# Performance work log

Measured on AMD Instinct MI355X. Metric: run time of the kernel, lower is better.

The kernel has to match this reference:

```python
import jax, jax.numpy as jnp
import numpy as np

N = 50000
E = 1600000
D_IN = 512   # embedding_num - 1
D_OUT = 512  # output1_dim


def setup_inputs() -> dict:
    key = jax.random.key(0)
    ks = jax.random.split(key, 16)
    A1_tensor = jax.random.normal(ks[0], (N, D_IN + 1), dtype=jnp.float32)
    adj_rows = jax.random.randint(ks[1], (E,), 0, N, dtype=jnp.int32)
    adj_cols = jax.random.randint(ks[2], (E,), 0, N, dtype=jnp.int32)
    adj_vals = jax.random.uniform(ks[3], (E,), dtype=jnp.float32)
    s = 1.0 / np.sqrt(D_IN)
    Lin1 = jax.random.uniform(ks[4], (D_IN, D_OUT), minval=-s, maxval=s, dtype=jnp.float32)
    Lin1_bias = jax.random.uniform(ks[5], (D_OUT,), minval=-s, maxval=s, dtype=jnp.float32)
    n = jax.random.uniform(ks[6], (N, 1), minval=0.0, maxval=1.0, dtype=jnp.float32)
    W1 = jax.random.uniform(ks[7], (D_IN, D_OUT), minval=-s, maxval=s, dtype=jnp.float32)
    b1 = jax.random.uniform(ks[8], (D_OUT,), minval=-s, maxval=s, dtype=jnp.float32)
    s2 = 1.0 / np.sqrt(D_OUT)
    W2 = jax.random.uniform(ks[9], (D_OUT, D_OUT), minval=-s2, maxval=s2, dtype=jnp.float32)
    b2 = jax.random.uniform(ks[10], (D_OUT,), minval=-s2, maxval=s2, dtype=jnp.float32)
    W3 = jax.random.uniform(ks[11], (D_OUT, D_OUT), minval=-s2, maxval=s2, dtype=jnp.float32)
    b3 = jax.random.uniform(ks[12], (D_OUT,), minval=-s2, maxval=s2, dtype=jnp.float32)
    return {"A1_tensor": A1_tensor, "adj_rows": adj_rows, "adj_cols": adj_cols,
            "adj_vals": adj_vals, "Lin1": Lin1, "Lin1_bias": Lin1_bias, "n": n,
            "W1": W1, "b1": b1, "W2": W2, "b2": b2, "W3": W3, "b3": b3}


def reference(A1_tensor, adj_rows, adj_cols, adj_vals, Lin1, Lin1_bias, n,
              W1, b1, W2, b2, W3, b3):
    num_nodes = A1_tensor.shape[0]

    def spmm(h):  # sparse adj @ h via edge-list gather + segment_sum
        return jax.ops.segment_sum(adj_vals[:, None] * h[adj_cols], adj_rows,
                                   num_segments=num_nodes)

    x = A1_tensor[:, 1:]                      # drop first feature column (dropout = identity at eval)
    a0 = x @ Lin1 + Lin1_bias                 # [N, D_OUT]
    a1 = a0 * n
    x1 = spmm(x @ W1 + b1)                    # gc1
    x1 = a1 + x1 * (1.0 - n)                  # gated blend
    x2 = spmm(x1 @ W2 + b2)                   # gc2
    x2 = spmm(x2 @ W3 + b3)                   # gc3
    return jnp.concatenate([x2, a0], axis=-1) # [N, 2*D_OUT]
```

## Files before the change

kernel.cpp:

```cpp
#include <hip/hip_runtime.h>
#include <stdint.h>

#define DD 512

typedef __bf16 bf16x8 __attribute__((ext_vector_type(8)));
typedef float f32x4 __attribute__((ext_vector_type(4)));

__device__ __forceinline__ unsigned short f2bf(float f) {
  uint32_t u = __builtin_bit_cast(uint32_t, f);
  u += 0x7fff + ((u >> 16) & 1);
  return (unsigned short)(u >> 16);
}
__device__ __forceinline__ float bfbits2f(uint32_t lo16) {
  return __builtin_bit_cast(float, lo16 << 16);
}

__global__ void hist_kernel(const int* __restrict__ rows, int* __restrict__ counts, int E) {
  int i = blockIdx.x * blockDim.x + threadIdx.x;
  if (i < E) atomicAdd(&counts[rows[i]], 1);
}

__global__ __launch_bounds__(256) void scan_block(const int* __restrict__ counts,
                                                  int* __restrict__ offs, int* __restrict__ bsum,
                                                  int n) {
  __shared__ int sm[256];
  int t = threadIdx.x;
  int i = blockIdx.x * 256 + t;
  int v = (i < n) ? ((counts[i] + 7) & ~7) : 0;
  sm[t] = v;
  __syncthreads();
  for (int o = 1; o < 256; o <<= 1) {
    int x = (t >= o) ? sm[t - o] : 0;
    __syncthreads();
    sm[t] += x;
    __syncthreads();
  }
  if (i < n) offs[i + 1] = sm[t];
  if (t == 255) bsum[blockIdx.x] = sm[255];
}

__global__ __launch_bounds__(256) void scan_tops(int* __restrict__ bsum, int nb) {
  __shared__ int sm[256];
  int t = threadIdx.x;
  int v = (t < nb) ? bsum[t] : 0;
  sm[t] = v;
  __syncthreads();
  for (int o = 1; o < 256; o <<= 1) {
    int x = (t >= o) ? sm[t - o] : 0;
    __syncthreads();
    sm[t] += x;
    __syncthreads();
  }
  if (t < nb) bsum[t] = sm[t];
}

__global__ __launch_bounds__(256) void scan_add(int* __restrict__ offs,
                                                const int* __restrict__ bsum, int n) {
  int i = blockIdx.x * 256 + threadIdx.x;
  int add = (blockIdx.x > 0) ? bsum[blockIdx.x - 1] : 0;
  if (i < n) offs[i + 1] += add;
  if (i == 0) offs[0] = 0;
}

__global__ void scatter_kernel(const int* __restrict__ rows, const int* __restrict__ colsIn,
                               const float* __restrict__ valsIn, const int* __restrict__ offs,
                               int* __restrict__ cursor, int* __restrict__ colsC,
                               unsigned short* __restrict__ valsC, int E) {
  int i = blockIdx.x * blockDim.x + threadIdx.x;
  if (i < E) {
    int r = rows[i];
    int p = offs[r] + atomicAdd(&cursor[r], 1);
    colsC[p] = colsIn[i];
    valsC[p] = f2bf(valsIn[i]);
  }
}

__global__ __launch_bounds__(256) void convert_x(const float* __restrict__ A1,
                                                 __bf16* __restrict__ Xb, int N) {
  int id = blockIdx.x * 256 + threadIdx.x;
  int total = (N * DD) >> 3;
  if (id >= total) return;
  int r = id >> 6;
  int c = (id & 63) * 8;
  const float* p = A1 + (size_t)r * 513 + 1 + c;
  unsigned short h[8];
#pragma unroll
  for (int k = 0; k < 8; ++k) h[k] = f2bf(p[k]);
  uint4 o;
  o.x = (uint32_t)h[0] | ((uint32_t)h[1] << 16);
  o.y = (uint32_t)h[2] | ((uint32_t)h[3] << 16);
  o.z = (uint32_t)h[4] | ((uint32_t)h[5] << 16);
  o.w = (uint32_t)h[6] | ((uint32_t)h[7] << 16);
  *(uint4*)(Xb + (size_t)r * DD + c) = o;
}

__global__ __launch_bounds__(256) void convert_wt(const float* __restrict__ W,
                                                  __bf16* __restrict__ Wt) {
  __shared__ float tile[32][33];
  int bx = blockIdx.x * 32;
  int by = blockIdx.y * 32;
  int tx = threadIdx.x & 31, ty = threadIdx.x >> 5;
#pragma unroll
  for (int q = 0; q < 4; ++q)
    tile[ty + q * 8][tx] = W[(size_t)(by + ty + q * 8) * DD + bx + tx];
  __syncthreads();
  unsigned short* Wts = (unsigned short*)Wt;
#pragma unroll
  for (int q = 0; q < 4; ++q)
    Wts[(size_t)(bx + ty + q * 8) * DD + by + tx] = f2bf(tile[tx][ty + q * 8]);
}

template <int MODE>
__global__ __launch_bounds__(256) void gemm_mfma(
    const __bf16* __restrict__ A,
    const __bf16* __restrict__ Bt,
    const float* __restrict__ bias,
    __bf16* __restrict__ Yb,
    float* __restrict__ out,
    const float* __restrict__ nvec,
    int M) {
  __shared__ __bf16 As[128][64];
  __shared__ __bf16 Bs[128][64];
  const int tid = threadIdx.x;
  const int bx = blockIdx.x >> 2;
  const int by = blockIdx.x & 3;
  const int bm = bx * 128;
  const int bn = by * 128;
  const int lane = tid & 63;
  const int w = tid >> 6;
  const int wm = (w & 1) * 64;
  const int wn = (w >> 1) * 64;
  const int m16 = lane & 15;
  const int quad = lane >> 4;

  f32x4 acc[4][4];
#pragma unroll
  for (int i = 0; i < 4; ++i)
#pragma unroll
    for (int j = 0; j < 4; ++j) acc[i][j] = (f32x4){0.f, 0.f, 0.f, 0.f};

  const int soff = tid * 16;
  const int srow_base = soff >> 7;
  const int skb = soff & 127;

  for (int k0 = 0; k0 < DD; k0 += 64) {
#pragma unroll
    for (int q = 0; q < 4; ++q) {
      int row = q * 32 + srow_base;
      int gm = bm + row;
      if (gm >= M) gm = M - 1;
      const char* ga = (const char*)A + ((size_t)gm * DD + k0) * 2 + skb;
      char* la = (char*)&As[0][0] + q * 4096 + w * 1024;
      __builtin_amdgcn_global_load_lds(
          (const __attribute__((address_space(1))) void*)ga,
          (__attribute__((address_space(3))) void*)la, 16, 0, 0);
      const char* gb = (const char*)Bt + ((size_t)(bn + row) * DD + k0) * 2 + skb;
      char* lb = (char*)&Bs[0][0] + q * 4096 + w * 1024;
      __builtin_amdgcn_global_load_lds(
          (const __attribute__((address_space(1))) void*)gb,
          (__attribute__((address_space(3))) void*)lb, 16, 0, 0);
    }
    __syncthreads();
#pragma unroll
    for (int ks = 0; ks < 2; ++ks) {
      int kb = ks * 32 + quad * 8;
      bf16x8 af[4], bf[4];
#pragma unroll
      for (int i = 0; i < 4; ++i) af[i] = *(const bf16x8*)&As[wm + i * 16 + m16][kb];
#pragma unroll
      for (int j = 0; j < 4; ++j) bf[j] = *(const bf16x8*)&Bs[wn + j * 16 + m16][kb];
#pragma unroll
      for (int i = 0; i < 4; ++i)
#pragma unroll
        for (int j = 0; j < 4; ++j)
          acc[i][j] = __builtin_amdgcn_mfma_f32_16x16x32_bf16(af[i], bf[j], acc[i][j], 0, 0, 0);
    }
    __syncthreads();
  }

  float bv[4];
#pragma unroll
  for (int j = 0; j < 4; ++j) bv[j] = bias[bn + wn + j * 16 + m16];

  unsigned short* Ybs = (unsigned short*)Yb;
#pragma unroll
  for (int i = 0; i < 4; ++i) {
#pragma unroll
    for (int r = 0; r < 4; ++r) {
      int row = bm + wm + i * 16 + quad * 4 + r;
      if (row < M) {
        if (MODE == 0) {
          float nv = nvec[row];
#pragma unroll
          for (int j = 0; j < 4; ++j) {
            int c = bn + wn + j * 16 + m16;
            float a0 = acc[i][j][r] + bv[j];
            out[(size_t)row * 1024 + 512 + c] = a0;
            out[(size_t)row * 1024 + c] = a0 * nv;
          }
        } else {
#pragma unroll
          for (int j = 0; j < 4; ++j) {
            int c = bn + wn + j * 16 + m16;
            Ybs[(size_t)row * DD + c] = f2bf(acc[i][j][r] + bv[j]);
          }
        }
      }
    }
  }
}

template <int MODE>
__global__ __launch_bounds__(256) void spmm_bf16(
    const int* __restrict__ offs, const int* __restrict__ cols,
    const unsigned short* __restrict__ vals,
    const __bf16* __restrict__ H,
    __bf16* __restrict__ Xb, float* __restrict__ outF,
    const float* __restrict__ a1, const float* __restrict__ nvec, int N) {
  int rg = threadIdx.x >> 7;
  int t = threadIdx.x & 127;
  int r = blockIdx.x * 2 + rg;
  if (r >= N) return;
  int d = t * 4;
  const unsigned short* Hp = (const unsigned short*)H + d;
  int s = offs[r], e = offs[r + 1];

  float ac0 = 0.f, ac1 = 0.f, ac2 = 0.f, ac3 = 0.f;
  for (int i = s; i < e; i += 8) {
    int4 ca = *(const int4*)(cols + i);
    int4 cb = *(const int4*)(cols + i + 4);
    uint4 vw = *(const uint4*)(vals + i);
    uint2 h[8];
    h[0] = *(const uint2*)(Hp + (size_t)ca.x * DD);
    h[1] = *(const uint2*)(Hp + (size_t)ca.y * DD);
    h[2] = *(const uint2*)(Hp + (size_t)ca.z * DD);
    h[3] = *(const uint2*)(Hp + (size_t)ca.w * DD);
    h[4] = *(const uint2*)(Hp + (size_t)cb.x * DD);
    h[5] = *(const uint2*)(Hp + (size_t)cb.y * DD);
    h[6] = *(const uint2*)(Hp + (size_t)cb.z * DD);
    h[7] = *(const uint2*)(Hp + (size_t)cb.w * DD);
    float v[8];
    v[0] = bfbits2f(vw.x & 0xffffu);
    v[1] = bfbits2f(vw.x >> 16);
    v[2] = bfbits2f(vw.y & 0xffffu);
    v[3] = bfbits2f(vw.y >> 16);
    v[4] = bfbits2f(vw.z & 0xffffu);
    v[5] = bfbits2f(vw.z >> 16);
    v[6] = bfbits2f(vw.w & 0xffffu);
    v[7] = bfbits2f(vw.w >> 16);
#pragma unroll
    for (int k = 0; k < 8; ++k) {
      ac0 += v[k] * bfbits2f(h[k].x & 0xffffu);
      ac1 += v[k] * bfbits2f(h[k].x >> 16);
      ac2 += v[k] * bfbits2f(h[k].y & 0xffffu);
      ac3 += v[k] * bfbits2f(h[k].y >> 16);
    }
  }

  if (MODE == 2) {
    float4 o;
    o.x = ac0; o.y = ac1; o.z = ac2; o.w = ac3;
    *(float4*)(outF + (size_t)r * 1024 + d) = o;
  } else {
    if (MODE == 1) {
      float g = 1.f - nvec[r];
      float4 a = *(const float4*)(a1 + (size_t)r * 1024 + d);
      ac0 = a.x + ac0 * g;
      ac1 = a.y + ac1 * g;
      ac2 = a.z + ac2 * g;
      ac3 = a.w + ac3 * g;
    }
    uint2 p;
    p.x = ((uint32_t)f2bf(ac1) << 16) | (uint32_t)f2bf(ac0);
    p.y = ((uint32_t)f2bf(ac3) << 16) | (uint32_t)f2bf(ac2);
    *(uint2*)((unsigned short*)Xb + (size_t)r * DD + d) = p;
  }
}

extern "C" void kernel_launch(void* const* d_in, const int* in_sizes, int n_in,
                              void* d_out, int out_size, void* d_ws, size_t ws_size,
                              hipStream_t stream) {
  const float* A1       = (const float*)d_in[0];
  const int*   adj_rows = (const int*)d_in[1];
  const int*   adj_cols = (const int*)d_in[2];
  const float* adj_vals = (const float*)d_in[3];
  const float* Lin1     = (const float*)d_in[4];
  const float* Lin1b    = (const float*)d_in[5];
  const float* nvec     = (const float*)d_in[6];
  const float* W1       = (const float*)d_in[7];
  const float* b1       = (const float*)d_in[8];
  const float* W2       = (const float*)d_in[9];
  const float* b2       = (const float*)d_in[10];
  const float* W3       = (const float*)d_in[11];
  const float* b3       = (const float*)d_in[12];
  const int N = in_sizes[6];
  const int E = in_sizes[1];
  float* out = (float*)d_out;

  uint8_t* base = (uint8_t*)d_ws;
  size_t off = 0;
  auto take = [&](size_t bytes) -> void* {
    off = (off + 255) & ~(size_t)255;
    void* r = base + off;
    off += bytes;
    return r;
  };
  const size_t EP = (size_t)E + 8 * (size_t)N;
  __bf16* Xb     = (__bf16*)take((size_t)N * DD * 2);
  __bf16* Yb     = (__bf16*)take((size_t)N * DD * 2);
  __bf16* Wt     = (__bf16*)take((size_t)4 * DD * DD * 2);
  int*    colsC  = (int*)take(EP * sizeof(int));
  unsigned short* valsC = (unsigned short*)take(EP * 2);
  int*    offs   = (int*)take((size_t)(N + 1) * sizeof(int));
  int*    counts = (int*)take((size_t)N * sizeof(int));
  int*    bsum   = (int*)take(1024);
  (void)ws_size; (void)n_in; (void)out_size;

  __bf16* Wt0 = Wt;
  __bf16* Wt1 = Wt + (size_t)DD * DD;
  __bf16* Wt2 = Wt + (size_t)2 * DD * DD;
  __bf16* Wt3 = Wt + (size_t)3 * DD * DD;

  int eb = (E + 255) / 256;
  int nb = (N + 255) / 256;

  hipMemsetAsync(counts, 0, (size_t)N * sizeof(int), stream);
  hipMemsetAsync(colsC, 0, EP * sizeof(int), stream);
  hipMemsetAsync(valsC, 0, EP * 2, stream);
  hist_kernel<<<eb, 256, 0, stream>>>(adj_rows, counts, E);
  scan_block<<<nb, 256, 0, stream>>>(counts, offs, bsum, N);
  scan_tops<<<1, 256, 0, stream>>>(bsum, nb);
  scan_add<<<nb, 256, 0, stream>>>(offs, bsum, N);
  hipMemsetAsync(counts, 0, (size_t)N * sizeof(int), stream);
  scatter_kernel<<<eb, 256, 0, stream>>>(adj_rows, adj_cols, adj_vals, offs, counts,
                                         colsC, valsC, E);

  convert_x<<<(N * DD / 8 + 255) / 256, 256, 0, stream>>>(A1, Xb, N);
  dim3 wgrid(16, 16);
  convert_wt<<<wgrid, 256, 0, stream>>>(Lin1, Wt0);
  convert_wt<<<wgrid, 256, 0, stream>>>(W1, Wt1);
  convert_wt<<<wgrid, 256, 0, stream>>>(W2, Wt2);
  convert_wt<<<wgrid, 256, 0, stream>>>(W3, Wt3);

  int ggrid = ((N + 127) / 128) * 4;
  int sgrid = (N + 1) / 2;

  gemm_mfma<0><<<ggrid, 256, 0, stream>>>(Xb, Wt0, Lin1b, nullptr, out, nvec, N);
  gemm_mfma<1><<<ggrid, 256, 0, stream>>>(Xb, Wt1, b1, Yb, nullptr, nullptr, N);
  spmm_bf16<1><<<sgrid, 256, 0, stream>>>(offs, colsC, valsC, Yb, Xb, nullptr, out, nvec, N);
  gemm_mfma<1><<<ggrid, 256, 0, stream>>>(Xb, Wt2, b2, Yb, nullptr, nullptr, N);
  spmm_bf16<0><<<sgrid, 256, 0, stream>>>(offs, colsC, valsC, Yb, Xb, nullptr, nullptr, nullptr, N);
  gemm_mfma<1><<<ggrid, 256, 0, stream>>>(Xb, Wt3, b3, Yb, nullptr, nullptr, N);
  spmm_bf16<2><<<sgrid, 256, 0, stream>>>(offs, colsC, valsC, Yb, nullptr, out, nullptr, nullptr, N);
}
```

Measured before the change: 1.381 ms.

## Bucket CSR columns by column range and widen SpMM rows to one wavefront

CSR construction now counts edges per (row, column-bucket) with 25 buckets of 2048 columns. Within each row, edges are scattered in bucket order, so the gathers of H rows are roughly sorted by column, which should improve L2 locality. The SpMM kernel now maps one 64-lane wavefront per row, with each lane loading 8 bf16 values (16 bytes) instead of 4. This gives wider gathers and 4 rows per block. In exchange, preprocessing gains extra kernels, a larger N*25 count array and its memsets, and more atomic contention in the scatter.

```diff
diff --git a/kernel.cpp b/kernel.cpp
--- a/kernel.cpp
+++ b/kernel.cpp
@@ -2,6 +2,8 @@
 #include <stdint.h>
 
 #define DD 512
+#define NB 25
+#define BSH 11
 
 typedef __bf16 bf16x8 __attribute__((ext_vector_type(8)));
 typedef float f32x4 __attribute__((ext_vector_type(4)));
@@ -15,9 +17,24 @@
   return __builtin_bit_cast(float, lo16 << 16);
 }
 
-__global__ void hist_kernel(const int* __restrict__ rows, int* __restrict__ counts, int E) {
+__global__ void hist2_kernel(const int* __restrict__ rows, const int* __restrict__ cols,
+                             int* __restrict__ counts2, int E) {
   int i = blockIdx.x * blockDim.x + threadIdx.x;
-  if (i < E) atomicAdd(&counts[rows[i]], 1);
+  if (i < E) {
+    int r = rows[i];
+    int b = cols[i] >> BSH;
+    atomicAdd(&counts2[r * NB + b], 1);
+  }
+}
+
+__global__ __launch_bounds__(256) void rowsum_kernel(const int* __restrict__ counts2,
+                                                     int* __restrict__ rowcnt, int n) {
+  int r = blockIdx.x * 256 + threadIdx.x;
+  if (r >= n) return;
+  int s = 0;
+#pragma unroll
+  for (int b = 0; b < NB; ++b) s += counts2[r * NB + b];
+  rowcnt[r] = s;
 }
 
 __global__ __launch_bounds__(256) void scan_block(const int* __restrict__ counts,
@@ -62,15 +79,31 @@
   if (i == 0) offs[0] = 0;
 }
 
-__global__ void scatter_kernel(const int* __restrict__ rows, const int* __restrict__ colsIn,
-                               const float* __restrict__ valsIn, const int* __restrict__ offs,
-                               int* __restrict__ cursor, int* __restrict__ colsC,
-                               unsigned short* __restrict__ valsC, int E) {
+__global__ __launch_bounds__(256) void bucketoff_kernel(const int* __restrict__ offs,
+                                                        const int* __restrict__ counts2,
+                                                        int* __restrict__ boff, int n) {
+  int r = blockIdx.x * 256 + threadIdx.x;
+  if (r >= n) return;
+  int run = offs[r];
+#pragma unroll
+  for (int b = 0; b < NB; ++b) {
+    boff[r * NB + b] = run;
+    run += counts2[r * NB + b];
+  }
+}
+
+__global__ void scatter2_kernel(const int* __restrict__ rows, const int* __restrict__ colsIn,
+                                const float* __restrict__ valsIn,
+                                const int* __restrict__ boff, int* __restrict__ cursor,
+                                int* __restrict__ colsC, unsigned short* __restrict__ valsC,
+                                int E) {
   int i = blockIdx.x * blockDim.x + threadIdx.x;
   if (i < E) {
     int r = rows[i];
-    int p = offs[r] + atomicAdd(&cursor[r], 1);
-    colsC[p] = colsIn[i];
+    int c = colsIn[i];
+    int b = c >> BSH;
+    int p = boff[r * NB + b] + atomicAdd(&cursor[r * NB + b], 1);
+    colsC[p] = c;
     valsC[p] = f2bf(valsIn[i]);
   }
 }
@@ -217,28 +250,31 @@
     const __bf16* __restrict__ H,
     __bf16* __restrict__ Xb, float* __restrict__ outF,
     const float* __restrict__ a1, const float* __restrict__ nvec, int N) {
-  int rg = threadIdx.x >> 7;
-  int t = threadIdx.x & 127;
-  int r = blockIdx.x * 2 + rg;
+  int rg = threadIdx.x >> 6;
+  int lane = threadIdx.x & 63;
+  int r = blockIdx.x * 4 + rg;
   if (r >= N) return;
-  int d = t * 4;
+  int d = lane * 8;
   const unsigned short* Hp = (const unsigned short*)H + d;
   int s = offs[r], e = offs[r + 1];
 
-  float ac0 = 0.f, ac1 = 0.f, ac2 = 0.f, ac3 = 0.f;
+  float ac[8];
+#pragma unroll
+  for (int k = 0; k < 8; ++k) ac[k] = 0.f;
+
   for (int i = s; i < e; i += 8) {
     int4 ca = *(const int4*)(cols + i);
     int4 cb = *(const int4*)(cols + i + 4);
     uint4 vw = *(const uint4*)(vals + i);
-    uint2 h[8];
-    h[0] = *(const uint2*)(Hp + (size_t)ca.x * DD);
-    h[1] = *(const uint2*)(Hp + (size_t)ca.y * DD);
-    h[2] = *(const uint2*)(Hp + (size_t)ca.z * DD);
-    h[3] = *(const uint2*)(Hp + (size_t)ca.w * DD);
-    h[4] = *(const uint2*)(Hp + (size_t)cb.x * DD);
-    h[5] = *(const uint2*)(Hp + (size_t)cb.y * DD);
-    h[6] = *(const uint2*)(Hp + (size_t)cb.z * DD);
-    h[7] = *(const uint2*)(Hp + (size_t)cb.w * DD);
+    uint4 h[8];
+    h[0] = *(const uint4*)(Hp + (size_t)ca.x * DD);
+    h[1] = *(const uint4*)(Hp + (size_t)ca.y * DD);
+    h[2] = *(const uint4*)(Hp + (size_t)ca.z * DD);
+    h[3] = *(const uint4*)(Hp + (size_t)ca.w * DD);
+    h[4] = *(const uint4*)(Hp + (size_t)cb.x * DD);
+    h[5] = *(const uint4*)(Hp + (size_t)cb.y * DD);
+    h[6] = *(const uint4*)(Hp + (size_t)cb.z * DD);
+    h[7] = *(const uint4*)(Hp + (size_t)cb.w * DD);
     float v[8];
     v[0] = bfbits2f(vw.x & 0xffffu);
     v[1] = bfbits2f(vw.x >> 16);
@@ -250,30 +286,43 @@
     v[7] = bfbits2f(vw.w >> 16);
 #pragma unroll
     for (int k = 0; k < 8; ++k) {
-      ac0 += v[k] * bfbits2f(h[k].x & 0xffffu);
-      ac1 += v[k] * bfbits2f(h[k].x >> 16);
-      ac2 += v[k] * bfbits2f(h[k].y & 0xffffu);
-      ac3 += v[k] * bfbits2f(h[k].y >> 16);
+      ac[0] += v[k] * bfbits2f(h[k].x & 0xffffu);
+      ac[1] += v[k] * bfbits2f(h[k].x >> 16);
+      ac[2] += v[k] * bfbits2f(h[k].y & 0xffffu);
+      ac[3] += v[k] * bfbits2f(h[k].y >> 16);
+      ac[4] += v[k] * bfbits2f(h[k].z & 0xffffu);
+      ac[5] += v[k] * bfbits2f(h[k].z >> 16);
+      ac[6] += v[k] * bfbits2f(h[k].w & 0xffffu);
+      ac[7] += v[k] * bfbits2f(h[k].w >> 16);
     }
   }
 
   if (MODE == 2) {
-    float4 o;
-    o.x = ac0; o.y = ac1; o.z = ac2; o.w = ac3;
-    *(float4*)(outF + (size_t)r * 1024 + d) = o;
+    float4 o0, o1;
+    o0.x = ac[0]; o0.y = ac[1]; o0.z = ac[2]; o0.w = ac[3];
+    o1.x = ac[4]; o1.y = ac[5]; o1.z = ac[6]; o1.w = ac[7];
+    *(float4*)(outF + (size_t)r * 1024 + d) = o0;
+    *(float4*)(outF + (size_t)r * 1024 + d + 4) = o1;
   } else {
     if (MODE == 1) {
       float g = 1.f - nvec[r];
-      float4 a = *(const float4*)(a1 + (size_t)r * 1024 + d);
-      ac0 = a.x + ac0 * g;
-      ac1 = a.y + ac1 * g;
-      ac2 = a.z + ac2 * g;
-      ac3 = a.w + ac3 * g;
+      float4 a0 = *(const float4*)(a1 + (size_t)r * 1024 + d);
+      float4 a1v = *(const float4*)(a1 + (size_t)r * 1024 + d + 4);
+      ac[0] = a0.x + ac[0] * g;
+      ac[1] = a0.y + ac[1] * g;
+      ac[2] = a0.z + ac[2] * g;
+      ac[3] = a0.w + ac[3] * g;
+      ac[4] = a1v.x + ac[4] * g;
+      ac[5] = a1v.y + ac[5] * g;
+      ac[6] = a1v.z + ac[6] * g;
+      ac[7] = a1v.w + ac[7] * g;
     }
-    uint2 p;
-    p.x = ((uint32_t)f2bf(ac1) << 16) | (uint32_t)f2bf(ac0);
-    p.y = ((uint32_t)f2bf(ac3) << 16) | (uint32_t)f2bf(ac2);
-    *(uint2*)((unsigned short*)Xb + (size_t)r * DD + d) = p;
+    uint4 p;
+    p.x = ((uint32_t)f2bf(ac[1]) << 16) | (uint32_t)f2bf(ac[0]);
+    p.y = ((uint32_t)f2bf(ac[3]) << 16) | (uint32_t)f2bf(ac[2]);
+    p.z = ((uint32_t)f2bf(ac[5]) << 16) | (uint32_t)f2bf(ac[4]);
+    p.w = ((uint32_t)f2bf(ac[7]) << 16) | (uint32_t)f2bf(ac[6]);
+    *(uint4*)((unsigned short*)Xb + (size_t)r * DD + d) = p;
   }
 }
 
@@ -312,7 +361,9 @@
   int*    colsC  = (int*)take(EP * sizeof(int));
   unsigned short* valsC = (unsigned short*)take(EP * 2);
   int*    offs   = (int*)take((size_t)(N + 1) * sizeof(int));
-  int*    counts = (int*)take((size_t)N * sizeof(int));
+  int*    counts2= (int*)take((size_t)N * NB * sizeof(int));
+  int*    boff   = (int*)take((size_t)N * NB * sizeof(int));
+  int*    rowcnt = (int*)take((size_t)N * sizeof(int));
   int*    bsum   = (int*)take(1024);
   (void)ws_size; (void)n_in; (void)out_size;
 
@@ -324,16 +375,18 @@
   int eb = (E + 255) / 256;
   int nb = (N + 255) / 256;
 
-  hipMemsetAsync(counts, 0, (size_t)N * sizeof(int), stream);
+  hipMemsetAsync(counts2, 0, (size_t)N * NB * sizeof(int), stream);
   hipMemsetAsync(colsC, 0, EP * sizeof(int), stream);
   hipMemsetAsync(valsC, 0, EP * 2, stream);
-  hist_kernel<<<eb, 256, 0, stream>>>(adj_rows, counts, E);
-  scan_block<<<nb, 256, 0, stream>>>(counts, offs, bsum, N);
+  hist2_kernel<<<eb, 256, 0, stream>>>(adj_rows, adj_cols, counts2, E);
+  rowsum_kernel<<<nb, 256, 0, stream>>>(counts2, rowcnt, N);
+  scan_block<<<nb, 256, 0, stream>>>(rowcnt, offs, bsum, N);
   scan_tops<<<1, 256, 0, stream>>>(bsum, nb);
   scan_add<<<nb, 256, 0, stream>>>(offs, bsum, N);
-  hipMemsetAsync(counts, 0, (size_t)N * sizeof(int), stream);
-  scatter_kernel<<<eb, 256, 0, stream>>>(adj_rows, adj_cols, adj_vals, offs, counts,
-                                         colsC, valsC, E);
+  bucketoff_kernel<<<nb, 256, 0, stream>>>(offs, counts2, boff, N);
+  hipMemsetAsync(counts2, 0, (size_t)N * NB * sizeof(int), stream);
+  scatter2_kernel<<<eb, 256, 0, stream>>>(adj_rows, adj_cols, adj_vals, boff, counts2,
+                                          colsC, valsC, E);
 
   convert_x<<<(N * DD / 8 + 255) / 256, 256, 0, stream>>>(A1, Xb, N);
   dim3 wgrid(16, 16);
@@ -343,7 +396,7 @@
   convert_wt<<<wgrid, 256, 0, stream>>>(W3, Wt3);
 
   int ggrid = ((N + 127) / 128) * 4;
-  int sgrid = (N + 1) / 2;
+  int sgrid = (N + 3) / 4;
 
   gemm_mfma<0><<<ggrid, 256, 0, stream>>>(Xb, Wt0, Lin1b, nullptr, out, nvec, N);
   gemm_mfma<1><<<ggrid, 256, 0, stream>>>(Xb, Wt1, b1, Yb, nullptr, nullptr, N);
```

Result: slower. 1.410 ms (+2.1%).
